# Kernel tuning notes

Hardware: AMD Instinct MI355X
Metric: run time of the kernel (lower is better)

The kernel has to match this reference:

```python
import jax, jax.numpy as jnp
import numpy as np

B, S, D, H = 2, 2048, 2048, 16
DK = D // H  # 128
ROPE_BASE = 10000.0


def _rope_tables(seq_len, d_k, dtype=jnp.float32):
    # cos/sin of shape [1, S, 1, d_k], duplicated halves as in the torch module
    inv_freq = 1.0 / (ROPE_BASE ** (jnp.arange(0, d_k, 2, dtype=jnp.float32) / d_k))
    pos = jnp.arange(seq_len, dtype=jnp.float32)
    freqs = jnp.outer(pos, inv_freq)               # [S, d_k/2]
    cos = jnp.concatenate([jnp.cos(freqs), jnp.cos(freqs)], axis=-1)  # [S, d_k]
    sin = jnp.concatenate([jnp.sin(freqs), jnp.sin(freqs)], axis=-1)
    return cos[None, :, None, :].astype(dtype), sin[None, :, None, :].astype(dtype)


def _rotate_half(x):
    d = x.shape[-1]
    x1, x2 = x[..., : d // 2], x[..., d // 2 :]
    return jnp.concatenate([-x2, x1], axis=-1)


def setup_inputs() -> dict:
    key = jax.random.key(0)
    ks = jax.random.split(key, 5)
    scale = 1.0 / np.sqrt(D)
    x = jax.random.normal(ks[0], (B, S, D), dtype=jnp.float32)
    Wq = jax.random.normal(ks[1], (D, D), dtype=jnp.float32) * scale
    Wk = jax.random.normal(ks[2], (D, D), dtype=jnp.float32) * scale
    Wv = jax.random.normal(ks[3], (D, D), dtype=jnp.float32) * scale
    Wo = jax.random.normal(ks[4], (D, D), dtype=jnp.float32) * scale
    bq = jnp.zeros((D,), jnp.float32)
    bk = jnp.zeros((D,), jnp.float32)
    bv = jnp.zeros((D,), jnp.float32)
    bo = jnp.zeros((D,), jnp.float32)
    mask = jnp.tril(jnp.ones((S, S), dtype=bool))[None, None]  # causal [1,1,S,S]
    return {"x": x, "mask": mask, "Wq": Wq, "bq": bq, "Wk": Wk, "bk": bk,
            "Wv": Wv, "bv": bv, "Wo": Wo, "bo": bo}


def reference(x, mask, Wq, bq, Wk, bk, Wv, bv, Wo, bo):
    b, s, d = x.shape
    # torch nn.Linear: y = x @ W.T + b
    Q = (x @ Wq.T + bq).reshape(b, s, H, DK)
    K = (x @ Wk.T + bk).reshape(b, s, H, DK)
    V = (x @ Wv.T + bv).reshape(b, s, H, DK)
    cos, sin = _rope_tables(s, DK, x.dtype)
    Q = Q * cos + _rotate_half(Q) * sin
    K = K * cos + _rotate_half(K) * sin
    # [b, h, s, dk]
    Q = Q.transpose(0, 2, 1, 3)
    K = K.transpose(0, 2, 1, 3)
    V = V.transpose(0, 2, 1, 3)
    scores = jnp.einsum("bhqd,bhkd->bhqk", Q, K) / jnp.sqrt(jnp.asarray(DK, x.dtype))
    scores = jnp.where(mask, scores, jnp.asarray(-jnp.inf, x.dtype))
    attn = jax.nn.softmax(scores, axis=-1)
    out = jnp.einsum("bhqk,bhkd->bhqd", attn, V)
    out = out.transpose(0, 2, 1, 3).reshape(b, s, d)
    return out @ Wo.T + bo
```

## Files before the change

### kernel.cpp

```cpp
#include <hip/hip_runtime.h>

typedef unsigned short u16;
typedef __attribute__((ext_vector_type(8))) short short8;
typedef __attribute__((ext_vector_type(4))) float f32x4;
typedef __attribute__((ext_vector_type(4))) unsigned short u16x4;

__device__ __forceinline__ float bf2f(u16 h){
  unsigned u = ((unsigned)h) << 16; float f; __builtin_memcpy(&f, &u, 4); return f;
}
__device__ __forceinline__ u16 f2bf(float f){
  unsigned u; __builtin_memcpy(&u, &f, 4);
  unsigned r = u + 0x7fffu + ((u >> 16) & 1u);
  return (u16)(r >> 16);
}

__device__ __forceinline__ void glds16(const u16* g, u16* l){
  __builtin_amdgcn_global_load_lds(
      (const __attribute__((address_space(1))) unsigned int*)(const void*)g,
      (__attribute__((address_space(3))) unsigned int*)(void*)l, 16, 0, 0);
}

__global__ __launch_bounds__(256) void cvt_all(const float* __restrict__ x,
    const float* __restrict__ w0, const float* __restrict__ w1,
    const float* __restrict__ w2, const float* __restrict__ w3,
    u16* __restrict__ xb, u16* __restrict__ wb){
  int blk = blockIdx.x;
  const float* src; u16* dst; int i;
  if (blk < 8192){
    src = x; dst = xb; i = blk * 256 + threadIdx.x;
  } else {
    int b2 = blk - 8192;
    int which = b2 >> 12;
    src = (which == 0) ? w0 : (which == 1) ? w1 : (which == 2) ? w2 : w3;
    dst = wb + (size_t)which * 4194304;
    i = (b2 & 4095) * 256 + threadIdx.x;
  }
  float4 f = ((const float4*)src)[i];
  u16x4 o; o.x = f2bf(f.x); o.y = f2bf(f.y); o.z = f2bf(f.z); o.w = f2bf(f.w);
  ((u16x4*)dst)[i] = o;
}

__global__ __launch_bounds__(256, 4) void gemm_bt(
    const u16* __restrict__ A, const u16* __restrict__ Bm, int mode,
    u16* __restrict__ qws, u16* __restrict__ kws, u16* __restrict__ vws,
    const float* __restrict__ bq, const float* __restrict__ bk, const float* __restrict__ bv,
    float* __restrict__ outf, const float* __restrict__ bo)
{
  const int K = 2048;
  __shared__ __attribute__((aligned(16))) u16 As[128 * 64];
  __shared__ __attribute__((aligned(16))) u16 Bs[128 * 64];

  int tid = threadIdx.x, wave = tid >> 6, lane = tid & 63;
  int quad = lane >> 4, l15 = lane & 15;
  int wm = wave >> 1, wn = wave & 1;

  size_t rowA0 = (size_t)blockIdx.y * 128;
  size_t rowB0 = (size_t)blockIdx.x * 128;

  int lrow0 = tid >> 3;
  int c0 = (tid & 7) ^ (lrow0 & 7);
  const u16* gA = A  + (rowA0 + lrow0) * K + c0 * 8;
  const u16* gB = Bm + (rowB0 + lrow0) * K + c0 * 8;
  u16* lA = As + (size_t)(wave * 64) * 8;
  u16* lB = Bs + (size_t)(wave * 64) * 8;

  f32x4 acc[4][4];
  #pragma unroll
  for (int i = 0; i < 4; i++)
    #pragma unroll
    for (int j = 0; j < 4; j++) acc[i][j] = f32x4{0.f, 0.f, 0.f, 0.f};

  int aoff[4], boff[4];
  #pragma unroll
  for (int t = 0; t < 4; t++){
    int ra = wm * 64 + t * 16 + l15;
    aoff[t] = ra * 64 + ((quad ^ (ra & 7)) * 8);
    int rb = wn * 32 + (t >> 1) * 64 + (t & 1) * 16 + l15;
    boff[t] = rb * 64 + ((quad ^ (rb & 7)) * 8);
  }

  for (int k0 = 0; k0 < K; k0 += 64){
    __syncthreads();
    #pragma unroll
    for (int ri = 0; ri < 4; ri++){
      glds16(gA + ri * 65536, lA + ri * 2048);
      glds16(gB + ri * 65536, lB + ri * 2048);
    }
    gA += 64; gB += 64;
    __syncthreads();
    #pragma unroll
    for (int kk = 0; kk < 2; kk++){
      const int kx = kk * 32;
      short8 af[4], bfr[4];
      #pragma unroll
      for (int t = 0; t < 4; t++){
        af[t]  = *(const short8*)(As + (aoff[t] ^ kx));
        bfr[t] = *(const short8*)(Bs + (boff[t] ^ kx));
      }
      #pragma unroll
      for (int i = 0; i < 4; i++)
        #pragma unroll
        for (int j = 0; j < 4; j++)
          acc[i][j] = __builtin_amdgcn_mfma_f32_16x16x32_bf16(af[i], bfr[j], acc[i][j], 0, 0, 0);
    }
  }

  if (mode == 0){
    int col0 = (int)rowB0;
    int mat = col0 >> 11;
    int cm  = col0 & 2047;
    const float* bias = (mat == 0) ? bq : (mat == 1) ? bk : bv;
    int b  = (int)(rowA0 >> 11);
    int s0 = (int)(rowA0 & 2047);
    int h  = cm >> 7;
    size_t base = ((size_t)(b * 16 + h)) * 2048 * 128;
    if (mat == 2){
      #pragma unroll
      for (int j = 0; j < 4; j++){
        int d = wn * 32 + (j >> 1) * 64 + (j & 1) * 16 + l15;
        float bv_ = bias[cm + d];
        #pragma unroll
        for (int i = 0; i < 4; i++){
          int srow = s0 + wm * 64 + i * 16 + quad * 4;
          u16x4 pk;
          #pragma unroll
          for (int r = 0; r < 4; r++) pk[r] = f2bf(acc[i][j][r] + bv_);
          *(u16x4*)(vws + base + (size_t)d * 2048 + srow) = pk;
        }
      }
    } else {
      u16* dst = (mat == 0) ? qws : kws;
      #pragma unroll
      for (int jp = 0; jp < 2; jp++){
        int dlow = wn * 32 + jp * 16 + l15;
        float bias_lo = bias[cm + dlow];
        float bias_hi = bias[cm + dlow + 64];
        float invf = __expf(-0.14391156831212788f * (float)dlow);
        #pragma unroll
        for (int i = 0; i < 4; i++){
          int srow0 = s0 + wm * 64 + i * 16 + quad * 4;
          #pragma unroll
          for (int r = 0; r < 4; r++){
            float a  = acc[i][jp][r]     + bias_lo;
            float b2 = acc[i][jp + 2][r] + bias_hi;
            float th = (float)(srow0 + r) * invf;
            float sn, cs; __sincosf(th, &sn, &cs);
            size_t ro = base + (size_t)(srow0 + r) * 128;
            dst[ro + dlow]      = f2bf(a * cs - b2 * sn);
            dst[ro + dlow + 64] = f2bf(b2 * cs + a * sn);
          }
        }
      }
    }
  } else {
    int col0 = (int)rowB0;
    #pragma unroll
    for (int j = 0; j < 4; j++){
      int c = col0 + wn * 32 + (j >> 1) * 64 + (j & 1) * 16 + l15;
      float bo_ = bo[c];
      #pragma unroll
      for (int i = 0; i < 4; i++){
        int rg = (int)rowA0 + wm * 64 + i * 16 + quad * 4;
        #pragma unroll
        for (int r = 0; r < 4; r++)
          outf[(size_t)(rg + r) * 2048 + c] = acc[i][j][r] + bo_;
      }
    }
  }
}

__global__ __launch_bounds__(256) void flash(
    const u16* __restrict__ Q, const u16* __restrict__ Km, const u16* __restrict__ VT,
    u16* __restrict__ O)
{
  __shared__ __attribute__((aligned(16))) u16 Ks[2][64 * 128];
  __shared__ __attribute__((aligned(16))) u16 Vs[2][128 * 64];
  __shared__ __attribute__((aligned(16))) u16 PL[4 * 32 * 72];
  const float scale = 0.08838834764831845f;

  int bh = blockIdx.y;
  int pr = (int)blockIdx.x;
  int tid = threadIdx.x, wave = tid >> 6, lane = tid & 63;
  int quad = lane >> 4, l15 = lane & 15;

  const u16* Qb = Q  + (size_t)bh * 2048 * 128;
  const u16* Kb = Km + (size_t)bh * 2048 * 128;
  const u16* Vb = VT + (size_t)bh * 2048 * 128;
  u16* PW = PL + wave * (32 * 72);

  const u16* gKb[4]; const u16* gVb[4]; int lOff[4];
  #pragma unroll
  for (int r = 0; r < 4; r++){
    int ci = r * 256 + wave * 64 + lane;
    int krow = ci >> 4;
    int klog = (ci & 15) ^ (krow & 15);
    gKb[r] = Kb + (size_t)krow * 128 + klog * 8;
    int vd = ci >> 3;
    int vlog = (ci & 7) ^ (vd & 7);
    gVb[r] = Vb + (size_t)vd * 2048 + vlog * 8;
    lOff[r] = (r * 256 + wave * 64) * 8;
  }

  for (int phase = 0; phase < 2; phase++){
    int qtile = phase ? (15 - pr) : pr;
    int qw = qtile * 128 + wave * 32;

    short8 qf[2][4];
    #pragma unroll
    for (int m = 0; m < 2; m++){
      const u16* qr = Qb + (size_t)(qw + m * 16 + l15) * 128 + quad * 8;
      #pragma unroll
      for (int c = 0; c < 4; c++) qf[m][c] = *(const short8*)(qr + c * 32);
    }

    float mr[2][4], lr[2][4]; f32x4 o[2][8];
    #pragma unroll
    for (int m = 0; m < 2; m++)
      #pragma unroll
      for (int r = 0; r < 4; r++){ mr[m][r] = -1e30f; lr[m][r] = 0.f; }
    #pragma unroll
    for (int m = 0; m < 2; m++)
      #pragma unroll
      for (int blk = 0; blk < 8; blk++) o[m][blk] = f32x4{0.f, 0.f, 0.f, 0.f};

    int niter = (qtile + 1) * 2;

    __syncthreads();
    #pragma unroll
    for (int r = 0; r < 4; r++){
      glds16(gKb[r], Ks[0] + lOff[r]);
      glds16(gVb[r], Vs[0] + lOff[r]);
    }

    for (int it = 0; it < niter; it++){
      int k0 = it * 64;
      int buf = it & 1;
      __syncthreads();
      if (it + 1 < niter){
        int nb = buf ^ 1;
        #pragma unroll
        for (int r = 0; r < 4; r++){
          glds16(gKb[r] + (size_t)(k0 + 64) * 128, Ks[nb] + lOff[r]);
          glds16(gVb[r] + (k0 + 64),               Vs[nb] + lOff[r]);
        }
      }
      const u16* KsB = Ks[buf];
      const u16* VsB = Vs[buf];

      int rel = qw + 31 - k0;
      if (rel >= 0){
        int smax = rel >> 4; if (smax > 3) smax = 3;
        float sreg[2][4][4];
        #pragma unroll
        for (int t = 0; t < 4; t++){
          if (t <= smax){
            short8 kf[4];
            #pragma unroll
            for (int c = 0; c < 4; c++)
              kf[c] = *(const short8*)(KsB + (t * 16 + l15) * 128 + (((c * 4 + quad) ^ l15) * 8));
            #pragma unroll
            for (int m = 0; m < 2; m++){
              f32x4 a = f32x4{0.f, 0.f, 0.f, 0.f};
              #pragma unroll
              for (int c = 0; c < 4; c++)
                a = __builtin_amdgcn_mfma_f32_16x16x32_bf16(qf[m][c], kf[c], a, 0, 0, 0);
              int kvcol = k0 + t * 16 + l15;
              #pragma unroll
              for (int r = 0; r < 4; r++){
                float v = a[r] * scale;
                int row = qw + m * 16 + quad * 4 + r;
                if (kvcol > row) v = -1e30f;
                sreg[m][t][r] = v;
              }
            }
          }
        }
        float alpha[2][4];
        #pragma unroll
        for (int m = 0; m < 2; m++){
          #pragma unroll
          for (int r = 0; r < 4; r++){
            float x = sreg[m][0][r];
            #pragma unroll
            for (int t = 1; t < 4; t++) if (t <= smax) x = fmaxf(x, sreg[m][t][r]);
            x = fmaxf(x, __shfl_xor(x, 1));
            x = fmaxf(x, __shfl_xor(x, 2));
            x = fmaxf(x, __shfl_xor(x, 4));
            x = fmaxf(x, __shfl_xor(x, 8));
            float mn = fmaxf(mr[m][r], x);
            alpha[m][r] = __expf(mr[m][r] - mn);
            mr[m][r] = mn;
          }
        }
        float lsum[2][4];
        #pragma unroll
        for (int m = 0; m < 2; m++)
          #pragma unroll
          for (int r = 0; r < 4; r++) lsum[m][r] = 0.f;
        #pragma unroll
        for (int t = 0; t < 4; t++){
          if (t <= smax){
            #pragma unroll
            for (int m = 0; m < 2; m++)
              #pragma unroll
              for (int r = 0; r < 4; r++){
                float p = __expf(sreg[m][t][r] - mr[m][r]);
                lsum[m][r] += p;
                PW[(m * 16 + quad * 4 + r) * 72 + t * 16 + l15] = f2bf(p);
              }
          }
        }
        if (!(smax & 1)){
          #pragma unroll
          for (int m = 0; m < 2; m++)
            #pragma unroll
            for (int r = 0; r < 4; r++)
              PW[(m * 16 + quad * 4 + r) * 72 + (smax + 1) * 16 + l15] = 0;
        }
        #pragma unroll
        for (int m = 0; m < 2; m++)
          #pragma unroll
          for (int r = 0; r < 4; r++){
            float sv = lsum[m][r];
            sv += __shfl_xor(sv, 1); sv += __shfl_xor(sv, 2);
            sv += __shfl_xor(sv, 4); sv += __shfl_xor(sv, 8);
            lr[m][r] = lr[m][r] * alpha[m][r] + sv;
          }
        #pragma unroll
        for (int m = 0; m < 2; m++)
          #pragma unroll
          for (int blk = 0; blk < 8; blk++){
            o[m][blk][0] *= alpha[m][0]; o[m][blk][1] *= alpha[m][1];
            o[m][blk][2] *= alpha[m][2]; o[m][blk][3] *= alpha[m][3];
          }
        __builtin_amdgcn_s_waitcnt(0xC07F);
        int nch = (smax >> 1) + 1;
        #pragma unroll
        for (int c2 = 0; c2 < 2; c2++){
          if (c2 < nch){
            short8 pf[2];
            #pragma unroll
            for (int m = 0; m < 2; m++)
              pf[m] = *(const short8*)(PW + (m * 16 + l15) * 72 + c2 * 32 + quad * 8);
            #pragma unroll
            for (int blk = 0; blk < 8; blk++){
              int d = blk * 16 + l15;
              short8 vf = *(const short8*)(VsB + d * 64 + (((c2 * 4 + quad) ^ (l15 & 7)) * 8));
              #pragma unroll
              for (int m = 0; m < 2; m++)
                o[m][blk] = __builtin_amdgcn_mfma_f32_16x16x32_bf16(pf[m], vf, o[m][blk], 0, 0, 0);
            }
          }
        }
      }
    }

    int b = bh >> 4, h = bh & 15;
    #pragma unroll
    for (int m = 0; m < 2; m++){
      float inv[4];
      #pragma unroll
      for (int r = 0; r < 4; r++) inv[r] = 1.0f / lr[m][r];
      #pragma unroll
      for (int blk = 0; blk < 8; blk++){
        int d = h * 128 + blk * 16 + l15;
        #pragma unroll
        for (int r = 0; r < 4; r++){
          int srow = qw + m * 16 + quad * 4 + r;
          O[((size_t)(b * 2048 + srow)) * 2048 + d] = f2bf(o[m][blk][r] * inv[r]);
        }
      }
    }
  }
}

extern "C" void kernel_launch(void* const* d_in, const int* in_sizes, int n_in,
                              void* d_out, int out_size, void* d_ws, size_t ws_size,
                              hipStream_t stream)
{
  const float* x  = (const float*)d_in[0];
  const float* Wq = (const float*)d_in[2];
  const float* bq = (const float*)d_in[3];
  const float* Wk = (const float*)d_in[4];
  const float* bk = (const float*)d_in[5];
  const float* Wv = (const float*)d_in[6];
  const float* bv = (const float*)d_in[7];
  const float* Wo = (const float*)d_in[8];
  const float* bo = (const float*)d_in[9];
  float* out = (float*)d_out;

  char* ws = (char*)d_ws;
  u16* xb   = (u16*)(ws);
  u16* wcat = (u16*)(ws + 16777216);
  u16* wob  = (u16*)(ws + 41943040);
  u16* qws  = (u16*)(ws + 50331648);
  u16* kws  = (u16*)(ws + 67108864);
  u16* vws  = (u16*)(ws + 83886080);
  u16* attn = (u16*)(ws + 100663296);

  cvt_all<<<24576, 256, 0, stream>>>(x, Wq, Wk, Wv, Wo, xb, wcat);

  gemm_bt<<<dim3(48, 32), 256, 0, stream>>>(xb, wcat, 0, qws, kws, vws,
                                            bq, bk, bv, nullptr, nullptr);
  flash<<<dim3(8, 32), 256, 0, stream>>>(qws, kws, vws, attn);
  gemm_bt<<<dim3(16, 32), 256, 0, stream>>>(attn, wob, 1, nullptr, nullptr, nullptr,
                                            nullptr, nullptr, nullptr, out, bo);
}
```

Measured before the change: 417.7 us.

## Halve flash query tile to 64 rows and double grid for occupancy

The flash attention kernel now processes 64-row query tiles, 16 rows per wave instead of 32, and launches twice as many blocks (16x32), with causal pairing of tiles pr and 31-pr. The P scratch buffer uses an XOR swizzle in place of padding, and launch bounds request two blocks per SM to raise occupancy. Each block now loads K/V tiles for half as many queries, so shared-memory traffic per unit of compute roughly doubles. In exchange the work is spread across more CUs and latency hiding should improve.

```diff
diff --git a/kernel.cpp b/kernel.cpp
--- a/kernel.cpp
+++ b/kernel.cpp
@@ -169,13 +169,13 @@
   }
 }
 
-__global__ __launch_bounds__(256) void flash(
+__global__ __launch_bounds__(256, 2) void flash(
     const u16* __restrict__ Q, const u16* __restrict__ Km, const u16* __restrict__ VT,
     u16* __restrict__ O)
 {
   __shared__ __attribute__((aligned(16))) u16 Ks[2][64 * 128];
   __shared__ __attribute__((aligned(16))) u16 Vs[2][128 * 64];
-  __shared__ __attribute__((aligned(16))) u16 PL[4 * 32 * 72];
+  __shared__ __attribute__((aligned(16))) u16 PL[4 * 16 * 64];
   const float scale = 0.08838834764831845f;
 
   int bh = blockIdx.y;
@@ -186,50 +186,38 @@
   const u16* Qb = Q  + (size_t)bh * 2048 * 128;
   const u16* Kb = Km + (size_t)bh * 2048 * 128;
   const u16* Vb = VT + (size_t)bh * 2048 * 128;
-  u16* PW = PL + wave * (32 * 72);
-
-  const u16* gKb[4]; const u16* gVb[4]; int lOff[4];
-  #pragma unroll
-  for (int r = 0; r < 4; r++){
-    int ci = r * 256 + wave * 64 + lane;
-    int krow = ci >> 4;
-    int klog = (ci & 15) ^ (krow & 15);
-    gKb[r] = Kb + (size_t)krow * 128 + klog * 8;
-    int vd = ci >> 3;
-    int vlog = (ci & 7) ^ (vd & 7);
-    gVb[r] = Vb + (size_t)vd * 2048 + vlog * 8;
-    lOff[r] = (r * 256 + wave * 64) * 8;
-  }
+  u16* PW = PL + wave * (16 * 64);
+
+  int krow0 = tid >> 4;
+  const u16* gK0 = Kb + (size_t)krow0 * 128 + ((tid & 15) ^ (krow0 & 15)) * 8;
+  int vd0 = tid >> 3;
+  const u16* gV0 = Vb + (size_t)vd0 * 2048 + ((tid & 7) ^ (vd0 & 7)) * 8;
+  int lOff0 = wave * 512;
 
   for (int phase = 0; phase < 2; phase++){
-    int qtile = phase ? (15 - pr) : pr;
-    int qw = qtile * 128 + wave * 32;
-
-    short8 qf[2][4];
-    #pragma unroll
-    for (int m = 0; m < 2; m++){
-      const u16* qr = Qb + (size_t)(qw + m * 16 + l15) * 128 + quad * 8;
-      #pragma unroll
-      for (int c = 0; c < 4; c++) qf[m][c] = *(const short8*)(qr + c * 32);
-    }
-
-    float mr[2][4], lr[2][4]; f32x4 o[2][8];
-    #pragma unroll
-    for (int m = 0; m < 2; m++)
-      #pragma unroll
-      for (int r = 0; r < 4; r++){ mr[m][r] = -1e30f; lr[m][r] = 0.f; }
-    #pragma unroll
-    for (int m = 0; m < 2; m++)
-      #pragma unroll
-      for (int blk = 0; blk < 8; blk++) o[m][blk] = f32x4{0.f, 0.f, 0.f, 0.f};
-
-    int niter = (qtile + 1) * 2;
+    int qtile = phase ? (31 - pr) : pr;
+    int qw = qtile * 64 + wave * 16;
+
+    short8 qf[4];
+    {
+      const u16* qr = Qb + (size_t)(qw + l15) * 128 + quad * 8;
+      #pragma unroll
+      for (int c = 0; c < 4; c++) qf[c] = *(const short8*)(qr + c * 32);
+    }
+
+    float mr[4], lr[4]; f32x4 o[8];
+    #pragma unroll
+    for (int r = 0; r < 4; r++){ mr[r] = -1e30f; lr[r] = 0.f; }
+    #pragma unroll
+    for (int blk = 0; blk < 8; blk++) o[blk] = f32x4{0.f, 0.f, 0.f, 0.f};
+
+    int niter = qtile + 1;
 
     __syncthreads();
     #pragma unroll
     for (int r = 0; r < 4; r++){
-      glds16(gKb[r], Ks[0] + lOff[r]);
-      glds16(gVb[r], Vs[0] + lOff[r]);
+      glds16(gK0 + r * 2048,  Ks[0] + lOff0 + r * 2048);
+      glds16(gV0 + r * 65536, Vs[0] + lOff0 + r * 2048);
     }
 
     for (int it = 0; it < niter; it++){
@@ -240,135 +228,114 @@
         int nb = buf ^ 1;
         #pragma unroll
         for (int r = 0; r < 4; r++){
-          glds16(gKb[r] + (size_t)(k0 + 64) * 128, Ks[nb] + lOff[r]);
-          glds16(gVb[r] + (k0 + 64),               Vs[nb] + lOff[r]);
+          glds16(gK0 + (size_t)(k0 + 64) * 128 + r * 2048, Ks[nb] + lOff0 + r * 2048);
+          glds16(gV0 + (k0 + 64) + r * 65536,              Vs[nb] + lOff0 + r * 2048);
         }
       }
       const u16* KsB = Ks[buf];
       const u16* VsB = Vs[buf];
 
-      int rel = qw + 31 - k0;
-      if (rel >= 0){
-        int smax = rel >> 4; if (smax > 3) smax = 3;
-        float sreg[2][4][4];
-        #pragma unroll
-        for (int t = 0; t < 4; t++){
-          if (t <= smax){
-            short8 kf[4];
-            #pragma unroll
-            for (int c = 0; c < 4; c++)
-              kf[c] = *(const short8*)(KsB + (t * 16 + l15) * 128 + (((c * 4 + quad) ^ l15) * 8));
-            #pragma unroll
-            for (int m = 0; m < 2; m++){
-              f32x4 a = f32x4{0.f, 0.f, 0.f, 0.f};
-              #pragma unroll
-              for (int c = 0; c < 4; c++)
-                a = __builtin_amdgcn_mfma_f32_16x16x32_bf16(qf[m][c], kf[c], a, 0, 0, 0);
-              int kvcol = k0 + t * 16 + l15;
-              #pragma unroll
-              for (int r = 0; r < 4; r++){
-                float v = a[r] * scale;
-                int row = qw + m * 16 + quad * 4 + r;
-                if (kvcol > row) v = -1e30f;
-                sreg[m][t][r] = v;
-              }
-            }
+      int rel = qw + 15 - k0;
+      int smax = rel >> 4; if (smax > 3) smax = 3;
+      float sreg[4][4];
+      #pragma unroll
+      for (int t = 0; t < 4; t++){
+        if (t <= smax){
+          short8 kf[4];
+          #pragma unroll
+          for (int c = 0; c < 4; c++)
+            kf[c] = *(const short8*)(KsB + (t * 16 + l15) * 128 + (((c * 4 + quad) ^ l15) * 8));
+          f32x4 a = f32x4{0.f, 0.f, 0.f, 0.f};
+          #pragma unroll
+          for (int c = 0; c < 4; c++)
+            a = __builtin_amdgcn_mfma_f32_16x16x32_bf16(qf[c], kf[c], a, 0, 0, 0);
+          int kvcol = k0 + t * 16 + l15;
+          #pragma unroll
+          for (int r = 0; r < 4; r++){
+            float v = a[r] * scale;
+            int row = qw + quad * 4 + r;
+            if (kvcol > row) v = -1e30f;
+            sreg[t][r] = v;
           }
         }
-        float alpha[2][4];
-        #pragma unroll
-        for (int m = 0; m < 2; m++){
+      }
+      float alpha[4];
+      #pragma unroll
+      for (int r = 0; r < 4; r++){
+        float x = sreg[0][r];
+        #pragma unroll
+        for (int t = 1; t < 4; t++) if (t <= smax) x = fmaxf(x, sreg[t][r]);
+        x = fmaxf(x, __shfl_xor(x, 1));
+        x = fmaxf(x, __shfl_xor(x, 2));
+        x = fmaxf(x, __shfl_xor(x, 4));
+        x = fmaxf(x, __shfl_xor(x, 8));
+        float mn = fmaxf(mr[r], x);
+        alpha[r] = __expf(mr[r] - mn);
+        mr[r] = mn;
+      }
+      float lsum[4];
+      #pragma unroll
+      for (int r = 0; r < 4; r++) lsum[r] = 0.f;
+      #pragma unroll
+      for (int t = 0; t < 4; t++){
+        if (t <= smax){
+          int chi = t * 2 + (l15 >> 3);
           #pragma unroll
           for (int r = 0; r < 4; r++){
-            float x = sreg[m][0][r];
-            #pragma unroll
-            for (int t = 1; t < 4; t++) if (t <= smax) x = fmaxf(x, sreg[m][t][r]);
-            x = fmaxf(x, __shfl_xor(x, 1));
-            x = fmaxf(x, __shfl_xor(x, 2));
-            x = fmaxf(x, __shfl_xor(x, 4));
-            x = fmaxf(x, __shfl_xor(x, 8));
-            float mn = fmaxf(mr[m][r], x);
-            alpha[m][r] = __expf(mr[m][r] - mn);
-            mr[m][r] = mn;
+            float p = __expf(sreg[t][r] - mr[r]);
+            lsum[r] += p;
+            int row = quad * 4 + r;
+            PW[row * 64 + ((chi ^ (row & 7)) << 3) + (l15 & 7)] = f2bf(p);
           }
         }
-        float lsum[2][4];
-        #pragma unroll
-        for (int m = 0; m < 2; m++)
-          #pragma unroll
-          for (int r = 0; r < 4; r++) lsum[m][r] = 0.f;
-        #pragma unroll
-        for (int t = 0; t < 4; t++){
-          if (t <= smax){
-            #pragma unroll
-            for (int m = 0; m < 2; m++)
-              #pragma unroll
-              for (int r = 0; r < 4; r++){
-                float p = __expf(sreg[m][t][r] - mr[m][r]);
-                lsum[m][r] += p;
-                PW[(m * 16 + quad * 4 + r) * 72 + t * 16 + l15] = f2bf(p);
-              }
+      }
+      if (!(smax & 1)){
+        int chi = (smax + 1) * 2 + (l15 >> 3);
+        #pragma unroll
+        for (int r = 0; r < 4; r++){
+          int row = quad * 4 + r;
+          PW[row * 64 + ((chi ^ (row & 7)) << 3) + (l15 & 7)] = 0;
+        }
+      }
+      #pragma unroll
+      for (int r = 0; r < 4; r++){
+        float sv = lsum[r];
+        sv += __shfl_xor(sv, 1); sv += __shfl_xor(sv, 2);
+        sv += __shfl_xor(sv, 4); sv += __shfl_xor(sv, 8);
+        lr[r] = lr[r] * alpha[r] + sv;
+      }
+      #pragma unroll
+      for (int blk = 0; blk < 8; blk++){
+        o[blk][0] *= alpha[0]; o[blk][1] *= alpha[1];
+        o[blk][2] *= alpha[2]; o[blk][3] *= alpha[3];
+      }
+      __builtin_amdgcn_s_waitcnt(0xC07F);
+      int nch = (smax >> 1) + 1;
+      #pragma unroll
+      for (int c2 = 0; c2 < 2; c2++){
+        if (c2 < nch){
+          short8 pf = *(const short8*)(PW + l15 * 64 + (((c2 * 4 + quad) ^ (l15 & 7)) << 3));
+          #pragma unroll
+          for (int blk = 0; blk < 8; blk++){
+            int d = blk * 16 + l15;
+            short8 vf = *(const short8*)(VsB + d * 64 + (((c2 * 4 + quad) ^ (l15 & 7)) * 8));
+            o[blk] = __builtin_amdgcn_mfma_f32_16x16x32_bf16(pf, vf, o[blk], 0, 0, 0);
           }
         }
-        if (!(smax & 1)){
-          #pragma unroll
-          for (int m = 0; m < 2; m++)
-            #pragma unroll
-            for (int r = 0; r < 4; r++)
-              PW[(m * 16 + quad * 4 + r) * 72 + (smax + 1) * 16 + l15] = 0;
-        }
-        #pragma unroll
-        for (int m = 0; m < 2; m++)
-          #pragma unroll
-          for (int r = 0; r < 4; r++){
-            float sv = lsum[m][r];
-            sv += __shfl_xor(sv, 1); sv += __shfl_xor(sv, 2);
-            sv += __shfl_xor(sv, 4); sv += __shfl_xor(sv, 8);
-            lr[m][r] = lr[m][r] * alpha[m][r] + sv;
-          }
-        #pragma unroll
-        for (int m = 0; m < 2; m++)
-          #pragma unroll
-          for (int blk = 0; blk < 8; blk++){
-            o[m][blk][0] *= alpha[m][0]; o[m][blk][1] *= alpha[m][1];
-            o[m][blk][2] *= alpha[m][2]; o[m][blk][3] *= alpha[m][3];
-          }
-        __builtin_amdgcn_s_waitcnt(0xC07F);
-        int nch = (smax >> 1) + 1;
-        #pragma unroll
-        for (int c2 = 0; c2 < 2; c2++){
-          if (c2 < nch){
-            short8 pf[2];
-            #pragma unroll
-            for (int m = 0; m < 2; m++)
-              pf[m] = *(const short8*)(PW + (m * 16 + l15) * 72 + c2 * 32 + quad * 8);
-            #pragma unroll
-            for (int blk = 0; blk < 8; blk++){
-              int d = blk * 16 + l15;
-              short8 vf = *(const short8*)(VsB + d * 64 + (((c2 * 4 + quad) ^ (l15 & 7)) * 8));
-              #pragma unroll
-              for (int m = 0; m < 2; m++)
-                o[m][blk] = __builtin_amdgcn_mfma_f32_16x16x32_bf16(pf[m], vf, o[m][blk], 0, 0, 0);
-            }
-          }
-        }
       }
     }
 
     int b = bh >> 4, h = bh & 15;
-    #pragma unroll
-    for (int m = 0; m < 2; m++){
-      float inv[4];
-      #pragma unroll
-      for (int r = 0; r < 4; r++) inv[r] = 1.0f / lr[m][r];
-      #pragma unroll
-      for (int blk = 0; blk < 8; blk++){
-        int d = h * 128 + blk * 16 + l15;
-        #pragma unroll
-        for (int r = 0; r < 4; r++){
-          int srow = qw + m * 16 + quad * 4 + r;
-          O[((size_t)(b * 2048 + srow)) * 2048 + d] = f2bf(o[m][blk][r] * inv[r]);
-        }
+    float inv[4];
+    #pragma unroll
+    for (int r = 0; r < 4; r++) inv[r] = 1.0f / lr[r];
+    #pragma unroll
+    for (int blk = 0; blk < 8; blk++){
+      int d = h * 128 + blk * 16 + l15;
+      #pragma unroll
+      for (int r = 0; r < 4; r++){
+        int srow = qw + quad * 4 + r;
+        O[((size_t)(b * 2048 + srow)) * 2048 + d] = f2bf(o[blk][r] * inv[r]);
       }
     }
   }
@@ -402,7 +369,7 @@
 
   gemm_bt<<<dim3(48, 32), 256, 0, stream>>>(xb, wcat, 0, qws, kws, vws,
                                             bq, bk, bv, nullptr, nullptr);
-  flash<<<dim3(8, 32), 256, 0, stream>>>(qws, kws, vws, attn);
+  flash<<<dim3(16, 32), 256, 0, stream>>>(qws, kws, vws, attn);
   gemm_bt<<<dim3(16, 32), 256, 0, stream>>>(attn, wob, 1, nullptr, nullptr, nullptr,
                                             nullptr, nullptr, nullptr, out, bo);
 }
```

Measured after the change: 412.3 us. About the same (-1.3%).
